# Performance work log

Measured on AMD Instinct MI355X. Metric: run time of the kernel, lower is better.

Reference implementation:

```python
import jax, jax.numpy as jnp
import numpy as np

B, H, D, SIZE, S = 32, 16, 64, 262144, 1024
GAMMA = 0.99

def setup_inputs() -> dict:
    key = jax.random.key(0)
    k1, k2, k3, k4 = jax.random.split(key, 4)
    return {
        "query": jax.random.normal(k1, (B, H, D), jnp.float32),
        "key_store": jax.random.normal(k2, (SIZE, H, D), jnp.float32),
        "value_store": jax.random.normal(k3, (SIZE, H, D), jnp.float32),
        "logit_store": 0.1 * jax.random.normal(k4, (SIZE, H), jnp.float32),
    }

def _sample_indices(logit_store, batch, rng):
    # torch softmax over dim=0 (batch*head rows) => per-row weights over s are
    # w[s] proportional to exp(logit[s,h]) / sum_h' exp(logit[s,h'])
    logw = logit_store.T - jax.nn.logsumexp(logit_store, axis=1)[None, :]  # (H, SIZE)
    u = jax.random.uniform(rng, (batch,) + logw.shape, minval=1e-12, maxval=1.0)
    gumbel = -jnp.log(-jnp.log(u))
    # Gumbel top-k == sampling without replacement proportional to exp(logw)
    _, idx = jax.lax.top_k(logw[None] + gumbel, S)  # (B, H, S)
    return idx

def reference(query, key_store, value_store, logit_store):
    b, h, d = query.shape
    idx = _sample_indices(logit_store, b, jax.random.key(42))  # (B,H,S)
    hidx = jnp.arange(h)[None, :, None]  # (1,H,1) broadcasts against idx
    kst = key_store.transpose(1, 0, 2)   # (H, SIZE, D)
    vst = value_store.transpose(1, 0, 2)
    sk = kst[hidx, idx]  # (B,H,S,D) gathered sample keys
    sv = vst[hidx, idx]  # (B,H,S,D) gathered sample values
    attn = jax.nn.softmax(jnp.einsum('bhd,bhsd->bhs', query, sk) * (d ** -0.5), axis=-1)
    lerp_k = jnp.einsum('bhs,bhsd->bhd', attn, sk)
    lerp_v = jnp.einsum('bhs,bhsd->bhd', attn, sv)
    # scattered in-place store updates
    new_k = (1.0 - attn)[..., None] * sk + attn[..., None] * lerp_k[:, :, None, :]
    new_v = (1.0 - attn)[..., None] * sv + attn[..., None] * lerp_v[:, :, None, :]
    key_store_new = kst.at[hidx, idx].set(new_k).transpose(1, 0, 2)
    value_store_new = vst.at[hidx, idx].set(new_v).transpose(1, 0, 2)
    lst = logit_store.T  # (H, SIZE)
    new_l = GAMMA * lst[hidx, idx] + attn  # RHS uses gathered old logits (matches torch)
    logit_store_new = lst.at[hidx, idx].set(new_l).T
    return lerp_k, lerp_v, key_store_new, value_store_new, logit_store_new
```

## Files before the change

### kernel.cpp

```cpp
#include <hip/hip_runtime.h>
#include <stdint.h>

static constexpr int NB = 32, NH = 16, ND = 64, NS = 1024;
static constexpr int SZ = 262144;
static constexpr int NROW = NB * NH;

typedef float f32x4 __attribute__((ext_vector_type(4)));

__device__ __forceinline__ uint32_t rotl32(uint32_t x, int r) { return (x << r) | (x >> (32 - r)); }

__device__ __forceinline__ void tf2x32(uint32_t x0, uint32_t x1, uint32_t& o0, uint32_t& o1) {
  const uint32_t K1 = 42u, K2 = 0x1BD11BF0u;
  x1 += K1;
#define TFR(r) { x0 += x1; x1 = rotl32(x1, (r)); x1 ^= x0; }
  TFR(13) TFR(15) TFR(26) TFR(6)
  x0 += K1; x1 += K2 + 1u;
  TFR(17) TFR(29) TFR(16) TFR(24)
  x0 += K2; x1 += 2u;
  TFR(13) TFR(15) TFR(26) TFR(6)
  x1 += K1 + 3u;
  TFR(17) TFR(29) TFR(16) TFR(24)
  x0 += K1; x1 += K2 + 4u;
  TFR(13) TFR(15) TFR(26) TFR(6)
  x0 += K2; x1 += 5u;
#undef TFR
  o0 = x0; o1 = x1;
}

__device__ __forceinline__ uint32_t bits_of(uint32_t row, uint32_t s) {
  uint32_t o0, o1; tf2x32(0u, (row << 18) | s, o0, o1);
  return o0 ^ o1;
}

__device__ __forceinline__ float gumbel_precise(uint32_t row, uint32_t s) {
  uint32_t bits = bits_of(row, s);
  float f = __uint_as_float((bits >> 9) | 0x3f800000u) - 1.0f;
  float u = fmaxf(1e-12f, f + 1e-12f);
  float t = -logf(u);
  return -logf(t);
}

__device__ __forceinline__ float uf_of(uint32_t row, uint32_t s) {
  return __uint_as_float((bits_of(row, s) >> 9) | 0x3f800000u);
}

__device__ __forceinline__ uint32_t fkey(float v) {
  uint32_t u = __float_as_uint(v);
  return (u & 0x80000000u) ? ~u : (u | 0x80000000u);
}

__global__ void k_logw(const float* __restrict__ logit, float* __restrict__ logw,
                       float* __restrict__ wexp, float* __restrict__ outL,
                       int* __restrict__ winner, float* __restrict__ W) {
  __shared__ float sW[16];
  const int tid = threadIdx.x;
  if (tid < 16) sW[tid] = 0.f;
  __syncthreads();
  int s = blockIdx.x * 256 + tid;
  const float4* p = (const float4*)(logit + (size_t)s * NH);
  float4 a0 = p[0], a1 = p[1], a2 = p[2], a3 = p[3];
  float x[16] = {a0.x,a0.y,a0.z,a0.w, a1.x,a1.y,a1.z,a1.w,
                 a2.x,a2.y,a2.z,a2.w, a3.x,a3.y,a3.z,a3.w};
  float m = x[0];
#pragma unroll
  for (int h = 1; h < 16; ++h) m = fmaxf(m, x[h]);
  float acc = 0.f;
#pragma unroll
  for (int h = 0; h < 16; ++h) acc += expf(x[h] - m);
  float lse = logf(acc) + m;
  float wl[16];
#pragma unroll
  for (int h = 0; h < 16; ++h) {
    float lw = x[h] - lse;
    logw[(size_t)h * SZ + s] = lw;
    float e = expf(lw);
    wexp[(size_t)h * SZ + s] = e;
    wl[h] = e;
  }
#pragma unroll
  for (int h = 0; h < 16; ++h) {
    float v = wl[h];
#pragma unroll
    for (int off = 32; off; off >>= 1) v += __shfl_xor(v, off);
    if ((tid & 63) == 0) atomicAdd(&sW[h], v);
  }
  float4* q = (float4*)(outL + (size_t)s * NH);
  q[0] = a0; q[1] = a1; q[2] = a2; q[3] = a3;
  int4 mone = make_int4(-1, -1, -1, -1);
  int4* w = (int4*)(winner + (size_t)s * NH);
  w[0] = mone; w[1] = mone; w[2] = mone; w[3] = mone;
  __syncthreads();
  if (tid < 16) atomicAdd(&W[tid], sW[tid]);
}

__device__ __forceinline__ void find_thresh(const uint32_t* hist, int nbins, int chunk,
                                            uint32_t need, int* outT, int tid) {
  if (tid < 64) {
    int hi = nbins - 1 - tid * chunk;
    uint32_t csum = 0;
    for (int j = 0; j < chunk; ++j) csum += hist[hi - j];
    uint32_t inc = csum;
#pragma unroll
    for (int off = 1; off < 64; off <<= 1) {
      uint32_t t = (uint32_t)__shfl_up((int)inc, off);
      if (tid >= off) inc += t;
    }
    uint32_t pre = inc - csum;
    if (pre < need && inc >= need) {
      uint32_t cum = pre; int T = hi - chunk + 1;
      for (int j = 0; j < chunk; ++j) {
        int b = hi - j;
        if (cum + hist[b] >= need) { T = b; break; }
        cum += hist[b];
      }
      *outT = T;
    }
  }
}

#define MEGA_T 512
#define SEL_BLKS 512
#define COPY_BLKS 2048
#define NCAND 5120
__global__ void __launch_bounds__(MEGA_T, 8) k_mega(
    const float* __restrict__ logw, const float* __restrict__ wexp,
    const float* __restrict__ Wsum, const float* __restrict__ qin,
    const float* __restrict__ Kst, const float* __restrict__ Vst,
    int* __restrict__ idx_sel, float* __restrict__ attn_ws,
    float* __restrict__ lerp_k, float* __restrict__ lerp_v, int* __restrict__ winner,
    f32x4* __restrict__ oK4, f32x4* __restrict__ oV4) {
  const int bid = blockIdx.x;
  const int tid = threadIdx.x;

  if (bid >= SEL_BLKS) {
    const f32x4* K4 = (const f32x4*)Kst;
    const f32x4* V4 = (const f32x4*)Vst;
    const long base = (long)(bid - SEL_BLKS) * MEGA_T + tid;
    const long stride = (long)COPY_BLKS * MEGA_T;
    for (int r = 0; r < 16; ++r) {
      long i0 = base + (long)(4 * r) * stride;
      long i1 = i0 + stride, i2 = i0 + 2 * stride, i3 = i0 + 3 * stride;
      f32x4 k0 = __builtin_nontemporal_load(&K4[i0]);
      f32x4 k1 = __builtin_nontemporal_load(&K4[i1]);
      f32x4 k2 = __builtin_nontemporal_load(&K4[i2]);
      f32x4 k3 = __builtin_nontemporal_load(&K4[i3]);
      f32x4 v0 = __builtin_nontemporal_load(&V4[i0]);
      f32x4 v1 = __builtin_nontemporal_load(&V4[i1]);
      f32x4 v2 = __builtin_nontemporal_load(&V4[i2]);
      f32x4 v3 = __builtin_nontemporal_load(&V4[i3]);
      __builtin_nontemporal_store(k0, &oK4[i0]);
      __builtin_nontemporal_store(k1, &oK4[i1]);
      __builtin_nontemporal_store(k2, &oK4[i2]);
      __builtin_nontemporal_store(k3, &oK4[i3]);
      __builtin_nontemporal_store(v0, &oV4[i0]);
      __builtin_nontemporal_store(v1, &oV4[i1]);
      __builtin_nontemporal_store(v2, &oV4[i2]);
      __builtin_nontemporal_store(v3, &oV4[i3]);
    }
    return;
  }

  const int row = bid;
  const int h = row & 15, b = row >> 4;
  const float* lw = logw + (size_t)h * SZ;
  const f32x4* we4 = (const f32x4*)(wexp + (size_t)h * SZ);
  int* outrow = idx_sel + (size_t)row * NS;

  __shared__ union {
    struct {
      int      cidx[NCAND];
      uint32_t hist[2048];
      uint16_t candA[2048];
      uint16_t candB[256];
      uint16_t candC[64];
    } s;
    struct {
      int   sel_s[NS];
      float sc[NS];
      float red[MEGA_T];
      f32x4 pk4[8][16], pv4[8][16];
    } a;
  } u;
  __shared__ int ctl[8];
  __shared__ float sNB;

  if (tid == 0) {
    float Wh = Wsum[h];
    sNB = -4096.0f / Wh;
    ctl[1] = 0;
  }
  __syncthreads();
  const float nB = sNB;
  const float CThr = 1.9999996f;

  for (int g = tid; g < SZ / 4; g += MEGA_T) {
    f32x4 w4 = __builtin_nontemporal_load(&we4[g]);
    int s0 = g << 2;
    float u0 = uf_of(row, s0);
    float u1 = uf_of(row, s0 + 1);
    float u2 = uf_of(row, s0 + 2);
    float u3 = uf_of(row, s0 + 3);
    if (u0 >= fmaf(nB, w4.x, CThr)) { int p = atomicAdd(&ctl[1], 1); if (p < NCAND) u.s.cidx[p] = s0; }
    if (u1 >= fmaf(nB, w4.y, CThr)) { int p = atomicAdd(&ctl[1], 1); if (p < NCAND) u.s.cidx[p] = s0 + 1; }
    if (u2 >= fmaf(nB, w4.z, CThr)) { int p = atomicAdd(&ctl[1], 1); if (p < NCAND) u.s.cidx[p] = s0 + 2; }
    if (u3 >= fmaf(nB, w4.w, CThr)) { int p = atomicAdd(&ctl[1], 1); if (p < NCAND) u.s.cidx[p] = s0 + 3; }
  }
  __syncthreads();
  const int C = min(ctl[1], NCAND);

  for (int i = tid; i < 2048; i += MEGA_T) u.s.hist[i] = 0;
  if (tid == 0) { ctl[0] = 0; ctl[3] = 0; ctl[4] = 0; ctl[5] = 0; }
  __syncthreads();
  for (int ci = tid; ci < C; ci += MEGA_T) {
    int s = u.s.cidx[ci];
    uint32_t k = fkey(lw[s] + gumbel_precise(row, s));
    atomicAdd(&u.s.hist[k >> 21], 1u);
  }
  __syncthreads();
  find_thresh(u.s.hist, 2048, 32, (uint32_t)NS, &ctl[2], tid);
  __syncthreads();
  const int T0 = ctl[2];
  for (int ci = tid; ci < C; ci += MEGA_T) {
    int s = u.s.cidx[ci];
    uint32_t k = fkey(lw[s] + gumbel_precise(row, s));
    int bb = (int)(k >> 21);
    if (bb > T0)       { int p = atomicAdd(&ctl[0], 1); outrow[p] = s; }
    else if (bb == T0) { int c = atomicAdd(&ctl[3], 1); if (c < 2048) u.s.candA[c] = (uint16_t)ci; }
  }
  __syncthreads();
  const int CA = min(ctl[3], 2048);
  for (int i = tid; i < 2048; i += MEGA_T) u.s.hist[i] = 0;
  __syncthreads();
  for (int i = tid; i < CA; i += MEGA_T) {
    int s = u.s.cidx[u.s.candA[i]];
    uint32_t k = fkey(lw[s] + gumbel_precise(row, s));
    atomicAdd(&u.s.hist[(k >> 10) & 0x7FFu], 1u);
  }
  __syncthreads();
  find_thresh(u.s.hist, 2048, 32, (uint32_t)(NS - ctl[0]), &ctl[2], tid);
  __syncthreads();
  const int T1 = ctl[2];
  for (int i = tid; i < CA; i += MEGA_T) {
    int ci = u.s.candA[i];
    int s = u.s.cidx[ci];
    uint32_t k = fkey(lw[s] + gumbel_precise(row, s));
    int mid = (int)((k >> 10) & 0x7FFu);
    if (mid > T1)       { int p = atomicAdd(&ctl[0], 1); outrow[p] = s; }
    else if (mid == T1) { int c = atomicAdd(&ctl[4], 1); if (c < 256) u.s.candB[c] = (uint16_t)ci; }
  }
  __syncthreads();
  const int CB = min(ctl[4], 256);
  for (int i = tid; i < 1024; i += MEGA_T) u.s.hist[i] = 0;
  __syncthreads();
  for (int i = tid; i < CB; i += MEGA_T) {
    int s = u.s.cidx[u.s.candB[i]];
    uint32_t k = fkey(lw[s] + gumbel_precise(row, s));
    atomicAdd(&u.s.hist[k & 0x3FFu], 1u);
  }
  __syncthreads();
  find_thresh(u.s.hist, 1024, 16, (uint32_t)(NS - ctl[0]), &ctl[2], tid);
  __syncthreads();
  const int T2 = ctl[2];
  for (int i = tid; i < CB; i += MEGA_T) {
    int ci = u.s.candB[i];
    int s = u.s.cidx[ci];
    uint32_t k = fkey(lw[s] + gumbel_precise(row, s));
    int lo = (int)(k & 0x3FFu);
    if (lo > T2)       { int p = atomicAdd(&ctl[0], 1); outrow[p] = s; }
    else if (lo == T2) { int c = atomicAdd(&ctl[5], 1); if (c < 64) u.s.candC[c] = (uint16_t)ci; }
  }
  __syncthreads();
  if (tid == 0) {
    int need = NS - ctl[0];
    int cc = min(ctl[5], 64);
    for (int k = 0; k < need; ++k) {
      int best = 0x7fffffff, bi = 0;
      for (int j = 0; j < cc; ++j) { int s = u.s.cidx[u.s.candC[j]]; if (s < best) { best = s; bi = j; } }
      if (best == 0x7fffffff) best = 0;
      outrow[ctl[0] + k] = best;
      if (cc > 0) u.s.cidx[u.s.candC[bi]] = 0x7fffffff;
    }
  }
  __syncthreads();

  const f32x4* K4 = (const f32x4*)Kst;
  const f32x4* V4 = (const f32x4*)Vst;
  const int lane = tid & 63, wv = tid >> 6;
  const int sj = lane >> 3, dj = lane & 7;
  for (int i = tid; i < NS; i += MEGA_T) u.a.sel_s[i] = outrow[i];
  const f32x4* q4 = (const f32x4*)(qin + (size_t)row * ND);
  f32x4 qa = q4[dj * 2], qb = q4[dj * 2 + 1];
  __syncthreads();
  for (int it = 0; it < 16; it += 2) {
    int i1 = it * 64 + wv * 8 + sj;
    int i2 = i1 + 64;
    int x1 = u.a.sel_s[i1], x2 = u.a.sel_s[i2];
    size_t b1 = ((size_t)x1 * NH + h) * 16 + dj * 2;
    size_t b2 = ((size_t)x2 * NH + h) * 16 + dj * 2;
    f32x4 ka1 = K4[b1], kb1 = K4[b1 + 1];
    f32x4 ka2 = K4[b2], kb2 = K4[b2 + 1];
    float p1 = ka1.x*qa.x + ka1.y*qa.y + ka1.z*qa.z + ka1.w*qa.w
             + kb1.x*qb.x + kb1.y*qb.y + kb1.z*qb.z + kb1.w*qb.w;
    float p2 = ka2.x*qa.x + ka2.y*qa.y + ka2.z*qa.z + ka2.w*qa.w
             + kb2.x*qb.x + kb2.y*qb.y + kb2.z*qb.z + kb2.w*qb.w;
#pragma unroll
    for (int off = 1; off < 8; off <<= 1) { p1 += __shfl_xor(p1, off); p2 += __shfl_xor(p2, off); }
    if (dj == 0) { u.a.sc[i1] = p1 * 0.125f; u.a.sc[i2] = p2 * 0.125f; }
  }
  __syncthreads();
  float v1 = u.a.sc[tid], v2 = u.a.sc[tid + 512];
  u.a.red[tid] = fmaxf(v1, v2); __syncthreads();
  for (int s = 256; s; s >>= 1) { if (tid < s) u.a.red[tid] = fmaxf(u.a.red[tid], u.a.red[tid + s]); __syncthreads(); }
  float m = u.a.red[0]; __syncthreads();
  float e1 = expf(v1 - m), e2 = expf(v2 - m);
  u.a.red[tid] = e1 + e2; __syncthreads();
  for (int s = 256; s; s >>= 1) { if (tid < s) u.a.red[tid] += u.a.red[tid + s]; __syncthreads(); }
  float inv = 1.0f / u.a.red[0];
  float a1 = e1 * inv, a2 = e2 * inv;
  u.a.sc[tid] = a1; u.a.sc[tid + 512] = a2;
  attn_ws[(size_t)row * NS + tid] = a1;
  attn_ws[(size_t)row * NS + tid + 512] = a2;
  __syncthreads();
  f32x4 AK = 0.f, BK = 0.f, AV = 0.f, BV = 0.f;
  for (int it = 0; it < 16; it += 2) {
    int i1 = it * 64 + wv * 8 + sj;
    int i2 = i1 + 64;
    int x1 = u.a.sel_s[i1], x2 = u.a.sel_s[i2];
    float c1 = u.a.sc[i1], c2 = u.a.sc[i2];
    size_t b1 = ((size_t)x1 * NH + h) * 16 + dj * 2;
    size_t b2 = ((size_t)x2 * NH + h) * 16 + dj * 2;
    f32x4 k1a = K4[b1], k1b = K4[b1 + 1], v1a = V4[b1], v1b = V4[b1 + 1];
    f32x4 k2a = K4[b2], k2b = K4[b2 + 1], v2a = V4[b2], v2b = V4[b2 + 1];
    AK += c1 * k1a + c2 * k2a; BK += c1 * k1b + c2 * k2b;
    AV += c1 * v1a + c2 * v2a; BV += c1 * v1b + c2 * v2b;
  }
#pragma unroll
  for (int off = 8; off < 64; off <<= 1) {
    AK.x += __shfl_xor(AK.x, off); AK.y += __shfl_xor(AK.y, off);
    AK.z += __shfl_xor(AK.z, off); AK.w += __shfl_xor(AK.w, off);
    BK.x += __shfl_xor(BK.x, off); BK.y += __shfl_xor(BK.y, off);
    BK.z += __shfl_xor(BK.z, off); BK.w += __shfl_xor(BK.w, off);
    AV.x += __shfl_xor(AV.x, off); AV.y += __shfl_xor(AV.y, off);
    AV.z += __shfl_xor(AV.z, off); AV.w += __shfl_xor(AV.w, off);
    BV.x += __shfl_xor(BV.x, off); BV.y += __shfl_xor(BV.y, off);
    BV.z += __shfl_xor(BV.z, off); BV.w += __shfl_xor(BV.w, off);
  }
  if (sj == 0) {
    u.a.pk4[wv][dj * 2] = AK; u.a.pk4[wv][dj * 2 + 1] = BK;
    u.a.pv4[wv][dj * 2] = AV; u.a.pv4[wv][dj * 2 + 1] = BV;
  }
  __syncthreads();
  if (tid < 64) {
    float lk = 0.f, lv = 0.f;
    const float* pkf = (const float*)u.a.pk4;
    const float* pvf = (const float*)u.a.pv4;
#pragma unroll
    for (int ww = 0; ww < 8; ++ww) { lk += pkf[ww * 64 + tid]; lv += pvf[ww * 64 + tid]; }
    lerp_k[(size_t)row * ND + tid] = lk;
    lerp_v[(size_t)row * ND + tid] = lv;
  }
  for (int i = tid; i < NS; i += MEGA_T) atomicMax(&winner[(size_t)u.a.sel_s[i] * NH + h], b);
}

__global__ void __launch_bounds__(256) k_fixup(const float* __restrict__ Kst,
    const float* __restrict__ Vst, const float* __restrict__ Lst,
    const int* __restrict__ idx_sel, const float* __restrict__ attn_ws,
    const int* __restrict__ winner, const float* __restrict__ lerp_k,
    const float* __restrict__ lerp_v, float* __restrict__ outK,
    float* __restrict__ outV, float* __restrict__ outL) {
  int g = blockIdx.x * 4 + (threadIdx.x >> 6);
  int lane = threadIdx.x & 63;
  int row = g >> 10, i = g & 1023;
  int h = row & 15, b = row >> 4;
  int idx = idx_sel[(size_t)row * NS + i];
  size_t slot = (size_t)idx * NH + h;
  if (winner[slot] != b) return;
  float a = attn_ws[(size_t)row * NS + i];
  size_t base = slot * ND + lane;
  float kv = Kst[base], vv = Vst[base];
  float lk = lerp_k[(size_t)row * ND + lane], lv = lerp_v[(size_t)row * ND + lane];
  float o = 1.0f - a;
  outK[base] = o * kv + a * lk;
  outV[base] = o * vv + a * lv;
  if (lane == 0) outL[slot] = 0.99f * Lst[slot] + a;
}

extern "C" void kernel_launch(void* const* d_in, const int* in_sizes, int n_in,
                              void* d_out, int out_size, void* d_ws, size_t ws_size,
                              hipStream_t stream) {
  const float* q   = (const float*)d_in[0];
  const float* Kst = (const float*)d_in[1];
  const float* Vst = (const float*)d_in[2];
  const float* Lst = (const float*)d_in[3];

  float* out    = (float*)d_out;
  float* out_lk = out;
  float* out_lv = out + 32768;
  float* outK   = out + 65536;
  float* outV   = outK + 268435456;
  float* outL   = outV + 268435456;

  char* ws = (char*)d_ws;
  float* logw   = (float*)ws;
  float* wexp   = (float*)(ws + (16ull << 20));
  int*   idxsel = (int*)(ws + (32ull << 20));
  float* attn   = (float*)(ws + (34ull << 20));
  int*   winner = (int*)(ws + (36ull << 20));
  float* Wsum   = (float*)(ws + (52ull << 20));

  hipMemsetAsync(Wsum, 0, 16 * sizeof(float), stream);
  k_logw<<<SZ / 256, 256, 0, stream>>>(Lst, logw, wexp, outL, winner, Wsum);
  k_mega<<<SEL_BLKS + COPY_BLKS, MEGA_T, 0, stream>>>(logw, wexp, Wsum, q, Kst, Vst,
                                                      idxsel, attn, out_lk, out_lv, winner,
                                                      (f32x4*)outK, (f32x4*)outV);
  k_fixup<<<NROW * NS / 4, 256, 0, stream>>>(Kst, Vst, Lst, idxsel, attn, winner,
                                             out_lk, out_lv, outK, outV, outL);
}
```

Measured before the change: 1.247 ms.

## Fuse scatter fixup into full store copy pass after selection

Removes the store-copy blocks from the selection mega-kernel and drops the per-sample fixup kernel. Selection and attention now run alone, then a small mark kernel records the winning attention weight per slot. An emit kernel streams the full key/value stores and applies the lerp update inline wherever a winner exists. This avoids a second scattered read/write pass over the updated slots, but it serializes the copy after selection where it previously overlapped, and it adds a winner read per 16-byte chunk.

New measurement: 1.333 ms. +6.9%, slower.

```diff
diff --git a/kernel.cpp b/kernel.cpp
--- a/kernel.cpp
+++ b/kernel.cpp
@@ -118,49 +118,16 @@
   }
 }
 
-#define MEGA_T 512
-#define SEL_BLKS 512
-#define COPY_BLKS 2048
+#define SEL_T 512
 #define NCAND 5120
-__global__ void __launch_bounds__(MEGA_T, 8) k_mega(
+__global__ void __launch_bounds__(SEL_T, 4) k_selattn(
     const float* __restrict__ logw, const float* __restrict__ wexp,
     const float* __restrict__ Wsum, const float* __restrict__ qin,
     const float* __restrict__ Kst, const float* __restrict__ Vst,
     int* __restrict__ idx_sel, float* __restrict__ attn_ws,
-    float* __restrict__ lerp_k, float* __restrict__ lerp_v, int* __restrict__ winner,
-    f32x4* __restrict__ oK4, f32x4* __restrict__ oV4) {
-  const int bid = blockIdx.x;
+    float* __restrict__ lerp_k, float* __restrict__ lerp_v, int* __restrict__ winner) {
+  const int row = blockIdx.x;
   const int tid = threadIdx.x;
-
-  if (bid >= SEL_BLKS) {
-    const f32x4* K4 = (const f32x4*)Kst;
-    const f32x4* V4 = (const f32x4*)Vst;
-    const long base = (long)(bid - SEL_BLKS) * MEGA_T + tid;
-    const long stride = (long)COPY_BLKS * MEGA_T;
-    for (int r = 0; r < 16; ++r) {
-      long i0 = base + (long)(4 * r) * stride;
-      long i1 = i0 + stride, i2 = i0 + 2 * stride, i3 = i0 + 3 * stride;
-      f32x4 k0 = __builtin_nontemporal_load(&K4[i0]);
-      f32x4 k1 = __builtin_nontemporal_load(&K4[i1]);
-      f32x4 k2 = __builtin_nontemporal_load(&K4[i2]);
-      f32x4 k3 = __builtin_nontemporal_load(&K4[i3]);
-      f32x4 v0 = __builtin_nontemporal_load(&V4[i0]);
-      f32x4 v1 = __builtin_nontemporal_load(&V4[i1]);
-      f32x4 v2 = __builtin_nontemporal_load(&V4[i2]);
-      f32x4 v3 = __builtin_nontemporal_load(&V4[i3]);
-      __builtin_nontemporal_store(k0, &oK4[i0]);
-      __builtin_nontemporal_store(k1, &oK4[i1]);
-      __builtin_nontemporal_store(k2, &oK4[i2]);
-      __builtin_nontemporal_store(k3, &oK4[i3]);
-      __builtin_nontemporal_store(v0, &oV4[i0]);
-      __builtin_nontemporal_store(v1, &oV4[i1]);
-      __builtin_nontemporal_store(v2, &oV4[i2]);
-      __builtin_nontemporal_store(v3, &oV4[i3]);
-    }
-    return;
-  }
-
-  const int row = bid;
   const int h = row & 15, b = row >> 4;
   const float* lw = logw + (size_t)h * SZ;
   const f32x4* we4 = (const f32x4*)(wexp + (size_t)h * SZ);
@@ -177,7 +144,7 @@
     struct {
       int   sel_s[NS];
       float sc[NS];
-      float red[MEGA_T];
+      float red[SEL_T];
       f32x4 pk4[8][16], pv4[8][16];
     } a;
   } u;
@@ -193,8 +160,8 @@
   const float nB = sNB;
   const float CThr = 1.9999996f;
 
-  for (int g = tid; g < SZ / 4; g += MEGA_T) {
-    f32x4 w4 = __builtin_nontemporal_load(&we4[g]);
+  for (int g = tid; g < SZ / 4; g += SEL_T) {
+    f32x4 w4 = we4[g];
     int s0 = g << 2;
     float u0 = uf_of(row, s0);
     float u1 = uf_of(row, s0 + 1);
@@ -208,10 +175,10 @@
   __syncthreads();
   const int C = min(ctl[1], NCAND);
 
-  for (int i = tid; i < 2048; i += MEGA_T) u.s.hist[i] = 0;
+  for (int i = tid; i < 2048; i += SEL_T) u.s.hist[i] = 0;
   if (tid == 0) { ctl[0] = 0; ctl[3] = 0; ctl[4] = 0; ctl[5] = 0; }
   __syncthreads();
-  for (int ci = tid; ci < C; ci += MEGA_T) {
+  for (int ci = tid; ci < C; ci += SEL_T) {
     int s = u.s.cidx[ci];
     uint32_t k = fkey(lw[s] + gumbel_precise(row, s));
     atomicAdd(&u.s.hist[k >> 21], 1u);
@@ -220,7 +187,7 @@
   find_thresh(u.s.hist, 2048, 32, (uint32_t)NS, &ctl[2], tid);
   __syncthreads();
   const int T0 = ctl[2];
-  for (int ci = tid; ci < C; ci += MEGA_T) {
+  for (int ci = tid; ci < C; ci += SEL_T) {
     int s = u.s.cidx[ci];
     uint32_t k = fkey(lw[s] + gumbel_precise(row, s));
     int bb = (int)(k >> 21);
@@ -229,9 +196,9 @@
   }
   __syncthreads();
   const int CA = min(ctl[3], 2048);
-  for (int i = tid; i < 2048; i += MEGA_T) u.s.hist[i] = 0;
-  __syncthreads();
-  for (int i = tid; i < CA; i += MEGA_T) {
+  for (int i = tid; i < 2048; i += SEL_T) u.s.hist[i] = 0;
+  __syncthreads();
+  for (int i = tid; i < CA; i += SEL_T) {
     int s = u.s.cidx[u.s.candA[i]];
     uint32_t k = fkey(lw[s] + gumbel_precise(row, s));
     atomicAdd(&u.s.hist[(k >> 10) & 0x7FFu], 1u);
@@ -240,7 +207,7 @@
   find_thresh(u.s.hist, 2048, 32, (uint32_t)(NS - ctl[0]), &ctl[2], tid);
   __syncthreads();
   const int T1 = ctl[2];
-  for (int i = tid; i < CA; i += MEGA_T) {
+  for (int i = tid; i < CA; i += SEL_T) {
     int ci = u.s.candA[i];
     int s = u.s.cidx[ci];
     uint32_t k = fkey(lw[s] + gumbel_precise(row, s));
@@ -250,9 +217,9 @@
   }
   __syncthreads();
   const int CB = min(ctl[4], 256);
-  for (int i = tid; i < 1024; i += MEGA_T) u.s.hist[i] = 0;
-  __syncthreads();
-  for (int i = tid; i < CB; i += MEGA_T) {
+  for (int i = tid; i < 1024; i += SEL_T) u.s.hist[i] = 0;
+  __syncthreads();
+  for (int i = tid; i < CB; i += SEL_T) {
     int s = u.s.cidx[u.s.candB[i]];
     uint32_t k = fkey(lw[s] + gumbel_precise(row, s));
     atomicAdd(&u.s.hist[k & 0x3FFu], 1u);
@@ -261,7 +228,7 @@
   find_thresh(u.s.hist, 1024, 16, (uint32_t)(NS - ctl[0]), &ctl[2], tid);
   __syncthreads();
   const int T2 = ctl[2];
-  for (int i = tid; i < CB; i += MEGA_T) {
+  for (int i = tid; i < CB; i += SEL_T) {
     int ci = u.s.candB[i];
     int s = u.s.cidx[ci];
     uint32_t k = fkey(lw[s] + gumbel_precise(row, s));
@@ -287,7 +254,7 @@
   const f32x4* V4 = (const f32x4*)Vst;
   const int lane = tid & 63, wv = tid >> 6;
   const int sj = lane >> 3, dj = lane & 7;
-  for (int i = tid; i < NS; i += MEGA_T) u.a.sel_s[i] = outrow[i];
+  for (int i = tid; i < NS; i += SEL_T) u.a.sel_s[i] = outrow[i];
   const f32x4* q4 = (const f32x4*)(qin + (size_t)row * ND);
   f32x4 qa = q4[dj * 2], qb = q4[dj * 2 + 1];
   __syncthreads();
@@ -359,30 +326,71 @@
     lerp_k[(size_t)row * ND + tid] = lk;
     lerp_v[(size_t)row * ND + tid] = lv;
   }
-  for (int i = tid; i < NS; i += MEGA_T) atomicMax(&winner[(size_t)u.a.sel_s[i] * NH + h], b);
-}
-
-__global__ void __launch_bounds__(256) k_fixup(const float* __restrict__ Kst,
-    const float* __restrict__ Vst, const float* __restrict__ Lst,
-    const int* __restrict__ idx_sel, const float* __restrict__ attn_ws,
-    const int* __restrict__ winner, const float* __restrict__ lerp_k,
-    const float* __restrict__ lerp_v, float* __restrict__ outK,
-    float* __restrict__ outV, float* __restrict__ outL) {
-  int g = blockIdx.x * 4 + (threadIdx.x >> 6);
-  int lane = threadIdx.x & 63;
-  int row = g >> 10, i = g & 1023;
-  int h = row & 15, b = row >> 4;
-  int idx = idx_sel[(size_t)row * NS + i];
+  for (int i = tid; i < NS; i += SEL_T) atomicMax(&winner[(size_t)u.a.sel_s[i] * NH + h], b);
+}
+
+__global__ void k_mark(const int* __restrict__ idx_sel, const float* __restrict__ attn_ws,
+                       const int* __restrict__ winner, const float* __restrict__ Lst,
+                       float* __restrict__ wa, float* __restrict__ outL) {
+  int t = blockIdx.x * 256 + threadIdx.x;
+  int row = t >> 10, h = row & 15, b = row >> 4;
+  int idx = idx_sel[t];
   size_t slot = (size_t)idx * NH + h;
-  if (winner[slot] != b) return;
-  float a = attn_ws[(size_t)row * NS + i];
-  size_t base = slot * ND + lane;
-  float kv = Kst[base], vv = Vst[base];
-  float lk = lerp_k[(size_t)row * ND + lane], lv = lerp_v[(size_t)row * ND + lane];
-  float o = 1.0f - a;
-  outK[base] = o * kv + a * lk;
-  outV[base] = o * vv + a * lv;
-  if (lane == 0) outL[slot] = 0.99f * Lst[slot] + a;
+  if (winner[slot] == b) {
+    float a = attn_ws[t];
+    wa[slot] = a;
+    outL[slot] = 0.99f * Lst[slot] + a;
+  }
+}
+
+__global__ void __launch_bounds__(256) k_emit(const f32x4* __restrict__ K4,
+    const f32x4* __restrict__ V4, const int* __restrict__ winner,
+    const float* __restrict__ wa, const f32x4* __restrict__ LK4,
+    const f32x4* __restrict__ LV4, f32x4* __restrict__ oK4, f32x4* __restrict__ oV4) {
+  const long base = (long)blockIdx.x * 256 + threadIdx.x;
+  const long stride = 8192L * 256;
+  for (int r = 0; r < 8; ++r) {
+    long i0 = base + (long)(4 * r) * stride;
+    long i1 = i0 + stride, i2 = i0 + 2 * stride, i3 = i0 + 3 * stride;
+    int s0 = (int)(i0 >> 4), s1 = (int)(i1 >> 4), s2 = (int)(i2 >> 4), s3 = (int)(i3 >> 4);
+    int w0 = winner[s0], w1 = winner[s1], w2 = winner[s2], w3 = winner[s3];
+    f32x4 k0 = __builtin_nontemporal_load(&K4[i0]);
+    f32x4 k1 = __builtin_nontemporal_load(&K4[i1]);
+    f32x4 k2 = __builtin_nontemporal_load(&K4[i2]);
+    f32x4 k3 = __builtin_nontemporal_load(&K4[i3]);
+    f32x4 v0 = __builtin_nontemporal_load(&V4[i0]);
+    f32x4 v1 = __builtin_nontemporal_load(&V4[i1]);
+    f32x4 v2 = __builtin_nontemporal_load(&V4[i2]);
+    f32x4 v3 = __builtin_nontemporal_load(&V4[i3]);
+    if (w0 >= 0) {
+      float a = wa[s0]; int rr = (w0 << 4) | (s0 & 15); float o = 1.0f - a;
+      k0 = o * k0 + a * LK4[((long)rr << 4) + (i0 & 15)];
+      v0 = o * v0 + a * LV4[((long)rr << 4) + (i0 & 15)];
+    }
+    if (w1 >= 0) {
+      float a = wa[s1]; int rr = (w1 << 4) | (s1 & 15); float o = 1.0f - a;
+      k1 = o * k1 + a * LK4[((long)rr << 4) + (i1 & 15)];
+      v1 = o * v1 + a * LV4[((long)rr << 4) + (i1 & 15)];
+    }
+    if (w2 >= 0) {
+      float a = wa[s2]; int rr = (w2 << 4) | (s2 & 15); float o = 1.0f - a;
+      k2 = o * k2 + a * LK4[((long)rr << 4) + (i2 & 15)];
+      v2 = o * v2 + a * LV4[((long)rr << 4) + (i2 & 15)];
+    }
+    if (w3 >= 0) {
+      float a = wa[s3]; int rr = (w3 << 4) | (s3 & 15); float o = 1.0f - a;
+      k3 = o * k3 + a * LK4[((long)rr << 4) + (i3 & 15)];
+      v3 = o * v3 + a * LV4[((long)rr << 4) + (i3 & 15)];
+    }
+    __builtin_nontemporal_store(k0, &oK4[i0]);
+    __builtin_nontemporal_store(k1, &oK4[i1]);
+    __builtin_nontemporal_store(k2, &oK4[i2]);
+    __builtin_nontemporal_store(k3, &oK4[i3]);
+    __builtin_nontemporal_store(v0, &oV4[i0]);
+    __builtin_nontemporal_store(v1, &oV4[i1]);
+    __builtin_nontemporal_store(v2, &oV4[i2]);
+    __builtin_nontemporal_store(v3, &oV4[i3]);
+  }
 }
 
 extern "C" void kernel_launch(void* const* d_in, const int* in_sizes, int n_in,
@@ -406,13 +414,15 @@
   int*   idxsel = (int*)(ws + (32ull << 20));
   float* attn   = (float*)(ws + (34ull << 20));
   int*   winner = (int*)(ws + (36ull << 20));
-  float* Wsum   = (float*)(ws + (52ull << 20));
+  float* wa     = (float*)(ws + (52ull << 20));
+  float* Wsum   = (float*)(ws + (68ull << 20));
 
   hipMemsetAsync(Wsum, 0, 16 * sizeof(float), stream);
   k_logw<<<SZ / 256, 256, 0, stream>>>(Lst, logw, wexp, outL, winner, Wsum);
-  k_mega<<<SEL_BLKS + COPY_BLKS, MEGA_T, 0, stream>>>(logw, wexp, Wsum, q, Kst, Vst,
-                                                      idxsel, attn, out_lk, out_lv, winner,
-                                                      (f32x4*)outK, (f32x4*)outV);
-  k_fixup<<<NROW * NS / 4, 256, 0, stream>>>(Kst, Vst, Lst, idxsel, attn, winner,
-                                             out_lk, out_lv, outK, outV, outL);
-}
+  k_selattn<<<NROW, SEL_T, 0, stream>>>(logw, wexp, Wsum, q, Kst, Vst,
+                                        idxsel, attn, out_lk, out_lv, winner);
+  k_mark<<<NROW * NS / 256, 256, 0, stream>>>(idxsel, attn, winner, Lst, wa, outL);
+  k_emit<<<8192, 256, 0, stream>>>((const f32x4*)Kst, (const f32x4*)Vst, winner, wa,
+                                   (const f32x4*)out_lk, (const f32x4*)out_lv,
+                                   (f32x4*)outK, (f32x4*)outV);
+}
```

## Split store copy, emitting the last quarter with fused in-place lerp updates

Applied to the files above, without the earlier changes.

The overlapped bulk copy in the mega kernel now covers only the first three quarters of the K/V stores. A new emit kernel streams the last quarter and applies the winner lerp update inline, so the fixup kernel only handles winners in the first three quarters. A new mark kernel writes the winning attention weights per slot and emits the logit update. The aim is to cut redundant scattered fixup reads and writes, at the cost of the last quarter of the copy no longer overlapping the selection work and two extra launches. The wexp load also becomes a regular cached load.

New measurement: 1.173 ms. -5.9%, faster.

```diff
diff --git a/kernel.cpp b/kernel.cpp
--- a/kernel.cpp
+++ b/kernel.cpp
@@ -4,6 +4,9 @@
 static constexpr int NB = 32, NH = 16, ND = 64, NS = 1024;
 static constexpr int SZ = 262144;
 static constexpr int NROW = NB * NH;
+static constexpr long N4 = 67108864L;
+static constexpr long SPLIT4 = 50331648L;
+static constexpr int SPLIT_IDX = 196608;
 
 typedef float f32x4 __attribute__((ext_vector_type(4)));
 
@@ -137,7 +140,7 @@
     const f32x4* V4 = (const f32x4*)Vst;
     const long base = (long)(bid - SEL_BLKS) * MEGA_T + tid;
     const long stride = (long)COPY_BLKS * MEGA_T;
-    for (int r = 0; r < 16; ++r) {
+    for (int r = 0; r < 12; ++r) {
       long i0 = base + (long)(4 * r) * stride;
       long i1 = i0 + stride, i2 = i0 + 2 * stride, i3 = i0 + 3 * stride;
       f32x4 k0 = __builtin_nontemporal_load(&K4[i0]);
@@ -194,7 +197,7 @@
   const float CThr = 1.9999996f;
 
   for (int g = tid; g < SZ / 4; g += MEGA_T) {
-    f32x4 w4 = __builtin_nontemporal_load(&we4[g]);
+    f32x4 w4 = we4[g];
     int s0 = g << 2;
     float u0 = uf_of(row, s0);
     float u1 = uf_of(row, s0 + 1);
@@ -343,7 +346,7 @@
     AV.x += __shfl_xor(AV.x, off); AV.y += __shfl_xor(AV.y, off);
     AV.z += __shfl_xor(AV.z, off); AV.w += __shfl_xor(AV.w, off);
     BV.x += __shfl_xor(BV.x, off); BV.y += __shfl_xor(BV.y, off);
-    BV.z += __shfl_xor(BV.z, off); BV.w += __shfl_xor(BV.w, off);
+    BV.w += __shfl_xor(BV.w, off); BV.z += __shfl_xor(BV.z, off);
   }
   if (sj == 0) {
     u.a.pk4[wv][dj * 2] = AK; u.a.pk4[wv][dj * 2 + 1] = BK;
@@ -362,17 +365,81 @@
   for (int i = tid; i < NS; i += MEGA_T) atomicMax(&winner[(size_t)u.a.sel_s[i] * NH + h], b);
 }
 
+__global__ void k_mark(const int* __restrict__ idx_sel, const float* __restrict__ attn_ws,
+                       const int* __restrict__ winner, const float* __restrict__ Lst,
+                       float* __restrict__ wa, float* __restrict__ outL) {
+  int t = blockIdx.x * 256 + threadIdx.x;
+  int row = t >> 10, h = row & 15, b = row >> 4;
+  int idx = idx_sel[t];
+  size_t slot = (size_t)idx * NH + h;
+  if (winner[slot] == b) {
+    float a = attn_ws[t];
+    wa[slot] = a;
+    outL[slot] = 0.99f * Lst[slot] + a;
+  }
+}
+
+__global__ void __launch_bounds__(512) k_emit2(const f32x4* __restrict__ K4,
+    const f32x4* __restrict__ V4, const int* __restrict__ winner,
+    const float* __restrict__ wa, const f32x4* __restrict__ LK4,
+    const f32x4* __restrict__ LV4, f32x4* __restrict__ oK4, f32x4* __restrict__ oV4) {
+  const long base = SPLIT4 + (long)blockIdx.x * 512 + threadIdx.x;
+  const long stride = 2048L * 512;
+  for (int r = 0; r < 4; ++r) {
+    long i0 = base + (long)(4 * r) * stride;
+    long i1 = i0 + stride, i2 = i0 + 2 * stride, i3 = i0 + 3 * stride;
+    int s0 = (int)(i0 >> 4), s1 = (int)(i1 >> 4), s2 = (int)(i2 >> 4), s3 = (int)(i3 >> 4);
+    int w0 = winner[s0], w1 = winner[s1], w2 = winner[s2], w3 = winner[s3];
+    f32x4 k0 = __builtin_nontemporal_load(&K4[i0]);
+    f32x4 k1 = __builtin_nontemporal_load(&K4[i1]);
+    f32x4 k2 = __builtin_nontemporal_load(&K4[i2]);
+    f32x4 k3 = __builtin_nontemporal_load(&K4[i3]);
+    f32x4 v0 = __builtin_nontemporal_load(&V4[i0]);
+    f32x4 v1 = __builtin_nontemporal_load(&V4[i1]);
+    f32x4 v2 = __builtin_nontemporal_load(&V4[i2]);
+    f32x4 v3 = __builtin_nontemporal_load(&V4[i3]);
+    if (w0 >= 0) {
+      float a = wa[s0]; int rr = (w0 << 4) | (s0 & 15); float o = 1.0f - a;
+      k0 = o * k0 + a * LK4[((long)rr << 4) + (i0 & 15)];
+      v0 = o * v0 + a * LV4[((long)rr << 4) + (i0 & 15)];
+    }
+    if (w1 >= 0) {
+      float a = wa[s1]; int rr = (w1 << 4) | (s1 & 15); float o = 1.0f - a;
+      k1 = o * k1 + a * LK4[((long)rr << 4) + (i1 & 15)];
+      v1 = o * v1 + a * LV4[((long)rr << 4) + (i1 & 15)];
+    }
+    if (w2 >= 0) {
+      float a = wa[s2]; int rr = (w2 << 4) | (s2 & 15); float o = 1.0f - a;
+      k2 = o * k2 + a * LK4[((long)rr << 4) + (i2 & 15)];
+      v2 = o * v2 + a * LV4[((long)rr << 4) + (i2 & 15)];
+    }
+    if (w3 >= 0) {
+      float a = wa[s3]; int rr = (w3 << 4) | (s3 & 15); float o = 1.0f - a;
+      k3 = o * k3 + a * LK4[((long)rr << 4) + (i3 & 15)];
+      v3 = o * v3 + a * LV4[((long)rr << 4) + (i3 & 15)];
+    }
+    __builtin_nontemporal_store(k0, &oK4[i0]);
+    __builtin_nontemporal_store(k1, &oK4[i1]);
+    __builtin_nontemporal_store(k2, &oK4[i2]);
+    __builtin_nontemporal_store(k3, &oK4[i3]);
+    __builtin_nontemporal_store(v0, &oV4[i0]);
+    __builtin_nontemporal_store(v1, &oV4[i1]);
+    __builtin_nontemporal_store(v2, &oV4[i2]);
+    __builtin_nontemporal_store(v3, &oV4[i3]);
+  }
+}
+
 __global__ void __launch_bounds__(256) k_fixup(const float* __restrict__ Kst,
-    const float* __restrict__ Vst, const float* __restrict__ Lst,
-    const int* __restrict__ idx_sel, const float* __restrict__ attn_ws,
-    const int* __restrict__ winner, const float* __restrict__ lerp_k,
-    const float* __restrict__ lerp_v, float* __restrict__ outK,
-    float* __restrict__ outV, float* __restrict__ outL) {
+    const float* __restrict__ Vst, const int* __restrict__ idx_sel,
+    const float* __restrict__ attn_ws, const int* __restrict__ winner,
+    const float* __restrict__ lerp_k, const float* __restrict__ lerp_v,
+    float* __restrict__ outK, float* __restrict__ outV) {
   int g = blockIdx.x * 4 + (threadIdx.x >> 6);
   int lane = threadIdx.x & 63;
   int row = g >> 10, i = g & 1023;
   int h = row & 15, b = row >> 4;
   int idx = idx_sel[(size_t)row * NS + i];
+  if (idx >= SPLIT_IDX) return;
   size_t slot = (size_t)idx * NH + h;
   if (winner[slot] != b) return;
   float a = attn_ws[(size_t)row * NS + i];
@@ -382,7 +449,6 @@
   float o = 1.0f - a;
   outK[base] = o * kv + a * lk;
   outV[base] = o * vv + a * lv;
-  if (lane == 0) outL[slot] = 0.99f * Lst[slot] + a;
 }
 
 extern "C" void kernel_launch(void* const* d_in, const int* in_sizes, int n_in,
@@ -406,13 +472,18 @@
   int*   idxsel = (int*)(ws + (32ull << 20));
   float* attn   = (float*)(ws + (34ull << 20));
   int*   winner = (int*)(ws + (36ull << 20));
-  float* Wsum   = (float*)(ws + (52ull << 20));
+  float* wa     = (float*)(ws + (52ull << 20));
+  float* Wsum   = (float*)(ws + (68ull << 20));
 
   hipMemsetAsync(Wsum, 0, 16 * sizeof(float), stream);
   k_logw<<<SZ / 256, 256, 0, stream>>>(Lst, logw, wexp, outL, winner, Wsum);
   k_mega<<<SEL_BLKS + COPY_BLKS, MEGA_T, 0, stream>>>(logw, wexp, Wsum, q, Kst, Vst,
                                                       idxsel, attn, out_lk, out_lv, winner,
                                                       (f32x4*)outK, (f32x4*)outV);
-  k_fixup<<<NROW * NS / 4, 256, 0, stream>>>(Kst, Vst, Lst, idxsel, attn, winner,
-                                             out_lk, out_lv, outK, outV, outL);
-}
+  k_mark<<<NROW * NS / 256, 256, 0, stream>>>(idxsel, attn, winner, Lst, wa, outL);
+  k_emit2<<<2048, 512, 0, stream>>>((const f32x4*)Kst, (const f32x4*)Vst, winner, wa,
+                                    (const f32x4*)out_lk, (const f32x4*)out_lv,
+                                    (f32x4*)outK, (f32x4*)outV);
+  k_fixup<<<NROW * NS / 4, 256, 0, stream>>>(Kst, Vst, idxsel, attn, winner,
+                                             out_lk, out_lv, outK, outV);
+}
```
